# Kernel tuning notes

Measured on AMD Instinct MI355X. Metric: run time of the kernel, lower is better.

The kernel has to match this reference:

```python
import jax, jax.numpy as jnp
import numpy as np

B, S, D, H = 8, 2048, 1024, 1024

def setup_inputs() -> dict:
    key = jax.random.key(0)
    ks = jax.random.split(key, 7)
    scale = 1.0 / np.sqrt(D)
    x = jax.random.normal(ks[0], (B, S, D), dtype=jnp.float32)
    W_q = jax.random.uniform(ks[1], (H, D), jnp.float32, -scale, scale)
    b_q = jax.random.uniform(ks[2], (H,), jnp.float32, -scale, scale)
    W_k = jax.random.uniform(ks[3], (H, D), jnp.float32, -scale, scale)
    b_k = jax.random.uniform(ks[4], (H,), jnp.float32, -scale, scale)
    W_v = jax.random.uniform(ks[5], (H, D), jnp.float32, -scale, scale)
    b_v = jax.random.uniform(ks[6], (H,), jnp.float32, -scale, scale)
    return {"x": x, "W_q": W_q, "b_q": b_q, "W_k": W_k, "b_k": b_k, "W_v": W_v, "b_v": b_v}

def reference(x, W_q, b_q, W_k, b_k, W_v, b_v):
    # Linear layers: y = x @ W.T + b (torch nn.Linear convention)
    q = jnp.einsum('bsd,hd->bsh', x, W_q) + b_q
    k = jnp.einsum('bsd,hd->bsh', x, W_k) + b_k
    v = jnp.einsum('bsd,hd->bsh', x, W_v) + b_v
    score = jnp.einsum('bqh,bkh->bqk', q, k) / jnp.sqrt(jnp.float32(H))
    causal = jnp.tril(jnp.ones((S, S), dtype=bool))  # lower-triangular mask
    score = jnp.where(causal, score, jnp.float32(-1e9))
    attn = jax.nn.softmax(score, axis=-1)
    return jnp.einsum('bqk,bkh->bqh', attn, v)
```

## Files before the change

kernel.cpp:

```cpp
#include <hip/hip_runtime.h>
#include <hip/hip_bf16.h>
#include <cstdint>

#define BB 8
#define SS 2048
#define DD 1024
#define HH 1024

typedef __bf16 bf16x8 __attribute__((ext_vector_type(8)));
typedef float f32x4 __attribute__((ext_vector_type(4)));

#define AS1C(p) ((const __attribute__((address_space(1))) void*)(p))
#define AS3(p)  ((__attribute__((address_space(3))) void*)(p))

__device__ __forceinline__ float bf2f(uint16_t h) {
  union { uint32_t u; float f; } v; v.u = ((uint32_t)h) << 16; return v.f;
}
__device__ __forceinline__ uint16_t f2bf(float f) {
  union { float f; uint32_t u; } v; v.f = f;
  uint32_t u = v.u;
  return (uint16_t)((u + 0x7FFFu + ((u >> 16) & 1u)) >> 16);
}

__global__ void cvt_f32_bf16(const float* __restrict__ src,
                             uint16_t* __restrict__ dst, int n) {
  int i = (blockIdx.x * blockDim.x + threadIdx.x) * 8;
  const int stride = gridDim.x * blockDim.x * 8;
  for (; i < n; i += stride) {
    float4 f0 = *(const float4*)(src + i);
    float4 f1 = *(const float4*)(src + i + 4);
    alignas(16) uint16_t o[8];
    o[0] = f2bf(f0.x); o[1] = f2bf(f0.y); o[2] = f2bf(f0.z); o[3] = f2bf(f0.w);
    o[4] = f2bf(f1.x); o[5] = f2bf(f1.y); o[6] = f2bf(f1.z); o[7] = f2bf(f1.w);
    *(uint4*)(dst + i) = *(const uint4*)o;
  }
}

__global__ void cvt3_f32_bf16(const float* __restrict__ s0, const float* __restrict__ s1,
                              const float* __restrict__ s2, uint16_t* __restrict__ d0,
                              uint16_t* __restrict__ d1, uint16_t* __restrict__ d2, int n) {
  const float* src = (blockIdx.y == 0) ? s0 : (blockIdx.y == 1) ? s1 : s2;
  uint16_t* dst = (blockIdx.y == 0) ? d0 : (blockIdx.y == 1) ? d1 : d2;
  int i = (blockIdx.x * blockDim.x + threadIdx.x) * 8;
  const int stride = gridDim.x * blockDim.x * 8;
  for (; i < n; i += stride) {
    float4 f0 = *(const float4*)(src + i);
    float4 f1 = *(const float4*)(src + i + 4);
    alignas(16) uint16_t o[8];
    o[0] = f2bf(f0.x); o[1] = f2bf(f0.y); o[2] = f2bf(f0.z); o[3] = f2bf(f0.w);
    o[4] = f2bf(f1.x); o[5] = f2bf(f1.y); o[6] = f2bf(f1.z); o[7] = f2bf(f1.w);
    *(uint4*)(dst + i) = *(const uint4*)o;
  }
}

template <int MODE>
__device__ __forceinline__ void gemm_body(const uint16_t* __restrict__ Aroot,
                                          const uint16_t* __restrict__ Broot,
                                          const float* __restrict__ bq,
                                          const float* __restrict__ bk,
                                          const float* __restrict__ bv,
                                          void* __restrict__ out0,
                                          uint16_t* __restrict__ out1,
                                          uint16_t* __restrict__ out2) {
  constexpr int K   = (MODE == 3) ? 2048 : 1024;
  constexpr int LDA = (MODE == 3) ? 2048 : 1024;
  constexpr int LDB = (MODE == 3) ? 2048 : 1024;

  const int tm = (MODE == 3) ? (gridDim.x - 1 - blockIdx.x) : blockIdx.x;
  const int tn = blockIdx.y;
  if constexpr (MODE == 2) { if (tn > tm) return; }

  const uint16_t* A = Aroot;
  const uint16_t* Bp = Broot;
  uint16_t* C16 = (uint16_t*)out0;
  float*    C32 = (float*)out0;
  if constexpr (MODE == 2) {
    size_t z = blockIdx.z;
    A  += z * (size_t)(SS * DD);
    Bp += z * (size_t)(SS * DD);
    C16 += z * (size_t)SS * (size_t)SS;
  }
  if constexpr (MODE == 3) {
    size_t z = blockIdx.z;
    A  += z * (size_t)SS * (size_t)SS;
    Bp += z * (size_t)(HH * SS);
    C32 += z * (size_t)(SS * HH);
  }

  const int m0 = tm * 128, n0 = tn * 128;
  int kmax = K;
  if constexpr (MODE == 3) {
    kmax = (tm + 1) * 128;
    if (kmax > K) kmax = K;
  }

  __shared__ uint16_t As0[128 * 32];
  __shared__ uint16_t As1[128 * 32];
  __shared__ uint16_t Bs0[128 * 32];
  __shared__ uint16_t Bs1[128 * 32];

  const int tid  = threadIdx.x;
  const int lane = tid & 63;
  const int wv   = tid >> 6;
  const int wm   = (wv & 1) * 64;
  const int wn   = (wv >> 1) * 64;

  f32x4 acc[4][4];
#pragma unroll
  for (int i = 0; i < 4; i++)
#pragma unroll
    for (int j = 0; j < 4; j++)
#pragma unroll
      for (int e = 0; e < 4; e++) acc[i][j][e] = 0.f;

  const int lrow = lane >> 2;
  const int lcol = (lane & 3) * 8;
  const int r0   = wv * 32;

  const uint16_t* gA = A + (size_t)(m0 + r0 + lrow) * LDA + lcol;
  const uint16_t* gB = Bp + (size_t)(n0 + r0 + lrow) * LDB + lcol;

  const int fr = lane & 15;
  const int fk = (lane >> 4) * 8;

  for (int k0 = 0; k0 < kmax; k0 += 64) {
    __syncthreads();
    __builtin_amdgcn_global_load_lds(AS1C(gA + k0), AS3(&As0[r0 * 32]), 16, 0, 0);
    __builtin_amdgcn_global_load_lds(AS1C(gA + k0 + 16 * LDA), AS3(&As0[(r0 + 16) * 32]), 16, 0, 0);
    __builtin_amdgcn_global_load_lds(AS1C(gA + k0 + 32), AS3(&As1[r0 * 32]), 16, 0, 0);
    __builtin_amdgcn_global_load_lds(AS1C(gA + k0 + 32 + 16 * LDA), AS3(&As1[(r0 + 16) * 32]), 16, 0, 0);
    __builtin_amdgcn_global_load_lds(AS1C(gB + k0), AS3(&Bs0[r0 * 32]), 16, 0, 0);
    __builtin_amdgcn_global_load_lds(AS1C(gB + k0 + 16 * LDB), AS3(&Bs0[(r0 + 16) * 32]), 16, 0, 0);
    __builtin_amdgcn_global_load_lds(AS1C(gB + k0 + 32), AS3(&Bs1[r0 * 32]), 16, 0, 0);
    __builtin_amdgcn_global_load_lds(AS1C(gB + k0 + 32 + 16 * LDB), AS3(&Bs1[(r0 + 16) * 32]), 16, 0, 0);
    __syncthreads();

    bf16x8 af[4], bfr[4];
#pragma unroll
    for (int i = 0; i < 4; i++)
      af[i] = __builtin_bit_cast(bf16x8, *(const uint4*)&As0[(wm + i * 16 + fr) * 32 + fk]);
#pragma unroll
    for (int j = 0; j < 4; j++)
      bfr[j] = __builtin_bit_cast(bf16x8, *(const uint4*)&Bs0[(wn + j * 16 + fr) * 32 + fk]);
#pragma unroll
    for (int i = 0; i < 4; i++)
#pragma unroll
      for (int j = 0; j < 4; j++)
        acc[i][j] = __builtin_amdgcn_mfma_f32_16x16x32_bf16(af[i], bfr[j], acc[i][j], 0, 0, 0);

#pragma unroll
    for (int i = 0; i < 4; i++)
      af[i] = __builtin_bit_cast(bf16x8, *(const uint4*)&As1[(wm + i * 16 + fr) * 32 + fk]);
#pragma unroll
    for (int j = 0; j < 4; j++)
      bfr[j] = __builtin_bit_cast(bf16x8, *(const uint4*)&Bs1[(wn + j * 16 + fr) * 32 + fk]);
#pragma unroll
    for (int i = 0; i < 4; i++)
#pragma unroll
      for (int j = 0; j < 4; j++)
        acc[i][j] = __builtin_amdgcn_mfma_f32_16x16x32_bf16(af[i], bfr[j], acc[i][j], 0, 0, 0);
  }

  const int cr = (lane >> 4) * 4;
  const int cc = lane & 15;

  if constexpr (MODE == 0) {
    const int sel   = n0 >> 10;
    const int nloc0 = n0 & 1023;
    const float* __restrict__ bsel = (sel == 0) ? bq : (sel == 1) ? bk : bv;
    uint16_t* __restrict__ oQK = (sel == 1) ? out1 : (uint16_t*)out0;
#pragma unroll
    for (int i = 0; i < 4; i++) {
#pragma unroll
      for (int j = 0; j < 4; j++) {
        const int row0 = m0 + wm + i * 16 + cr;
        const int coll = nloc0 + wn + j * 16 + cc;
        const float badd = bsel[coll];
#pragma unroll
        for (int e = 0; e < 4; e++) {
          const float x = acc[i][j][e] + badd;
          const int r = row0 + e;
          if (sel == 2) {
            const int bz = r >> 11;
            const int s  = r & (SS - 1);
            out2[(size_t)bz * (HH * SS) + (size_t)coll * SS + s] = f2bf(x);
          } else {
            oQK[(size_t)r * HH + coll] = f2bf(x);
          }
        }
      }
    }
  } else {
#pragma unroll
    for (int i = 0; i < 4; i++) {
#pragma unroll
      for (int j = 0; j < 4; j++) {
        const int row0 = m0 + wm + i * 16 + cr;
        const int col  = n0 + wn + j * 16 + cc;
#pragma unroll
        for (int e = 0; e < 4; e++) {
          float x = acc[i][j][e];
          const int r = row0 + e;
          if constexpr (MODE == 2) {
            C16[(size_t)r * SS + col] = f2bf(x * 0.03125f);
          } else {
            C32[(size_t)r * HH + col] = x;
          }
        }
      }
    }
  }
}

__launch_bounds__(256, 2)
__global__ void gemm_proj(const uint16_t* __restrict__ A, const uint16_t* __restrict__ B,
                          const float* __restrict__ bq, const float* __restrict__ bk,
                          const float* __restrict__ bv, void* __restrict__ o0,
                          uint16_t* __restrict__ o1, uint16_t* __restrict__ o2) {
  gemm_body<0>(A, B, bq, bk, bv, o0, o1, o2);
}
__launch_bounds__(256, 2)
__global__ void gemm_score(const uint16_t* __restrict__ A, const uint16_t* __restrict__ B,
                           void* __restrict__ o0) {
  gemm_body<2>(A, B, nullptr, nullptr, nullptr, o0, nullptr, nullptr);
}
__launch_bounds__(256, 2)
__global__ void gemm_pv(const uint16_t* __restrict__ A, const uint16_t* __restrict__ B,
                        void* __restrict__ o0) {
  gemm_body<3>(A, B, nullptr, nullptr, nullptr, o0, nullptr, nullptr);
}

__launch_bounds__(256)
__global__ void softmax_causal(uint16_t* __restrict__ Sb) {
  const int rgl = blockIdx.x;
  const int b = rgl >> 11;
  const int i = rgl & (SS - 1);
  uint16_t* row = Sb + (size_t)b * SS * SS + (size_t)i * SS;
  const int t = threadIdx.x;
  const int base = t * 8;
  const int cover = ((i >> 7) + 1) << 7;
  const bool act = base < cover;

  uint4 u; u.x = u.y = u.z = u.w = 0u;
  if (act) u = *(const uint4*)(row + base);
  const uint16_t* hs = (const uint16_t*)&u;
  float x[8];
  float lmax = -3.0e38f;
#pragma unroll
  for (int e = 0; e < 8; e++) {
    float f = bf2f(hs[e]);
    x[e] = (act && base + e <= i) ? f : -3.0e38f;
    lmax = fmaxf(lmax, x[e]);
  }
#pragma unroll
  for (int off = 32; off > 0; off >>= 1)
    lmax = fmaxf(lmax, __shfl_down(lmax, off));

  __shared__ float red[8];
  if ((t & 63) == 0) red[t >> 6] = lmax;
  __syncthreads();
  const float m = fmaxf(fmaxf(red[0], red[1]), fmaxf(red[2], red[3]));

  float lsum = 0.f;
#pragma unroll
  for (int e = 0; e < 8; e++) {
    float p = (act && base + e <= i) ? __expf(x[e] - m) : 0.f;
    x[e] = p;
    lsum += p;
  }
#pragma unroll
  for (int off = 32; off > 0; off >>= 1) lsum += __shfl_down(lsum, off);
  if ((t & 63) == 0) red[4 + (t >> 6)] = lsum;
  __syncthreads();
  const float inv = 1.f / (red[4] + red[5] + red[6] + red[7]);

  if (act) {
    alignas(16) uint16_t o[8];
#pragma unroll
    for (int e = 0; e < 8; e++) o[e] = f2bf(x[e] * inv);
    *(uint4*)(row + base) = *(const uint4*)o;
  }
}

extern "C" void kernel_launch(void* const* d_in, const int* in_sizes, int n_in,
                              void* d_out, int out_size, void* d_ws, size_t ws_size,
                              hipStream_t stream) {
  const float* x  = (const float*)d_in[0];
  const float* Wq = (const float*)d_in[1];
  const float* bq = (const float*)d_in[2];
  const float* Wk = (const float*)d_in[3];
  const float* bk = (const float*)d_in[4];
  const float* Wv = (const float*)d_in[5];
  const float* bv = (const float*)d_in[6];

  uint16_t* ws = (uint16_t*)d_ws;
  const size_t QKV = (size_t)BB * SS * HH;
  uint16_t* Q  = ws;
  uint16_t* Kp = ws + QKV;
  uint16_t* Vt = ws + 2 * QKV;
  uint16_t* Sb = ws + 3 * QKV;
  uint16_t* xb  = Sb;
  uint16_t* Wqb = Sb + QKV;
  uint16_t* Wkb = Wqb + (size_t)HH * DD;
  uint16_t* Wvb = Wkb + (size_t)HH * DD;

  dim3 blk(256);
  const int nx = BB * SS * DD;
  const int nw = HH * DD;
  cvt_f32_bf16<<<dim3(nx / 2048), blk, 0, stream>>>(x, xb, nx);
  cvt3_f32_bf16<<<dim3(nw / 2048, 3), blk, 0, stream>>>(Wq, Wk, Wv, Wqb, Wkb, Wvb, nw);

  gemm_proj<<<dim3(BB * SS / 128, 3 * HH / 128), blk, 0, stream>>>(
      xb, Wqb, bq, bk, bv, Q, Kp, Vt);
  gemm_score<<<dim3(SS / 128, SS / 128, BB), blk, 0, stream>>>(Q, Kp, Sb);
  softmax_causal<<<dim3(BB * SS), blk, 0, stream>>>(Sb);
  gemm_pv<<<dim3(SS / 128, HH / 128, BB), blk, 0, stream>>>(Sb, Vt, d_out);
}
```

Baseline: 419.8 us.

## Fuse causal softmax into score GEMM epilogue and PV normalization

Removes the separate softmax kernel. The score GEMM epilogue now writes exp(score) unnormalized, skipping max subtraction, and accumulates per-row sums with atomics; the PV GEMM divides by the row sum in its epilogue. This saves a full read/write pass over the B×S×S score matrix and one launch. It adds atomic traffic and a memset, and it drops the max subtraction, which risks overflow if the scores are large.

Result: no change. 416.0 us (-0.9%).

```diff
diff --git a/kernel.cpp b/kernel.cpp
--- a/kernel.cpp
+++ b/kernel.cpp
@@ -61,7 +61,8 @@
                                           const float* __restrict__ bv,
                                           void* __restrict__ out0,
                                           uint16_t* __restrict__ out1,
-                                          uint16_t* __restrict__ out2) {
+                                          uint16_t* __restrict__ out2,
+                                          float* __restrict__ rs) {
   constexpr int K   = (MODE == 3) ? 2048 : 1024;
   constexpr int LDA = (MODE == 3) ? 2048 : 1024;
   constexpr int LDB = (MODE == 3) ? 2048 : 1024;
@@ -79,12 +80,14 @@
     A  += z * (size_t)(SS * DD);
     Bp += z * (size_t)(SS * DD);
     C16 += z * (size_t)SS * (size_t)SS;
+    rs += z * (size_t)SS;
   }
   if constexpr (MODE == 3) {
     size_t z = blockIdx.z;
     A  += z * (size_t)SS * (size_t)SS;
     Bp += z * (size_t)(HH * SS);
     C32 += z * (size_t)(SS * HH);
+    rs += z * (size_t)SS;
   }
 
   const int m0 = tm * 128, n0 = tn * 128;
@@ -190,22 +193,40 @@
         }
       }
     }
+  } else if constexpr (MODE == 2) {
+#pragma unroll
+    for (int i = 0; i < 4; i++) {
+#pragma unroll
+      for (int e = 0; e < 4; e++) {
+        const int row = m0 + wm + i * 16 + cr + e;
+        float s = 0.f;
+#pragma unroll
+        for (int j = 0; j < 4; j++) {
+          const int col = n0 + wn + j * 16 + cc;
+          float p = (col <= row) ? __expf(acc[i][j][e] * 0.03125f) : 0.f;
+          const uint16_t pb = f2bf(p);
+          C16[(size_t)row * SS + col] = pb;
+          s += bf2f(pb);
+        }
+        s += __shfl_xor(s, 1);
+        s += __shfl_xor(s, 2);
+        s += __shfl_xor(s, 4);
+        s += __shfl_xor(s, 8);
+        if (cc == 0) atomicAdd(&rs[row], s);
+      }
+    }
   } else {
 #pragma unroll
     for (int i = 0; i < 4; i++) {
+      const int rr = m0 + wm + i * 16 + cr;
+      const float4 rv = *(const float4*)&rs[rr];
+      const float inv[4] = {1.f / rv.x, 1.f / rv.y, 1.f / rv.z, 1.f / rv.w};
 #pragma unroll
       for (int j = 0; j < 4; j++) {
-        const int row0 = m0 + wm + i * 16 + cr;
-        const int col  = n0 + wn + j * 16 + cc;
+        const int col = n0 + wn + j * 16 + cc;
 #pragma unroll
         for (int e = 0; e < 4; e++) {
-          float x = acc[i][j][e];
-          const int r = row0 + e;
-          if constexpr (MODE == 2) {
-            C16[(size_t)r * SS + col] = f2bf(x * 0.03125f);
-          } else {
-            C32[(size_t)r * HH + col] = x;
-          }
+          C32[(size_t)(rr + e) * HH + col] = acc[i][j][e] * inv[e];
         }
       }
     }
@@ -217,69 +238,17 @@
                           const float* __restrict__ bq, const float* __restrict__ bk,
                           const float* __restrict__ bv, void* __restrict__ o0,
                           uint16_t* __restrict__ o1, uint16_t* __restrict__ o2) {
-  gemm_body<0>(A, B, bq, bk, bv, o0, o1, o2);
+  gemm_body<0>(A, B, bq, bk, bv, o0, o1, o2, nullptr);
 }
 __launch_bounds__(256, 2)
 __global__ void gemm_score(const uint16_t* __restrict__ A, const uint16_t* __restrict__ B,
-                           void* __restrict__ o0) {
-  gemm_body<2>(A, B, nullptr, nullptr, nullptr, o0, nullptr, nullptr);
+                           void* __restrict__ o0, float* __restrict__ rs) {
+  gemm_body<2>(A, B, nullptr, nullptr, nullptr, o0, nullptr, nullptr, rs);
 }
 __launch_bounds__(256, 2)
 __global__ void gemm_pv(const uint16_t* __restrict__ A, const uint16_t* __restrict__ B,
-                        void* __restrict__ o0) {
-  gemm_body<3>(A, B, nullptr, nullptr, nullptr, o0, nullptr, nullptr);
-}
-
-__launch_bounds__(256)
-__global__ void softmax_causal(uint16_t* __restrict__ Sb) {
-  const int rgl = blockIdx.x;
-  const int b = rgl >> 11;
-  const int i = rgl & (SS - 1);
-  uint16_t* row = Sb + (size_t)b * SS * SS + (size_t)i * SS;
-  const int t = threadIdx.x;
-  const int base = t * 8;
-  const int cover = ((i >> 7) + 1) << 7;
-  const bool act = base < cover;
-
-  uint4 u; u.x = u.y = u.z = u.w = 0u;
-  if (act) u = *(const uint4*)(row + base);
-  const uint16_t* hs = (const uint16_t*)&u;
-  float x[8];
-  float lmax = -3.0e38f;
-#pragma unroll
-  for (int e = 0; e < 8; e++) {
-    float f = bf2f(hs[e]);
-    x[e] = (act && base + e <= i) ? f : -3.0e38f;
-    lmax = fmaxf(lmax, x[e]);
-  }
-#pragma unroll
-  for (int off = 32; off > 0; off >>= 1)
-    lmax = fmaxf(lmax, __shfl_down(lmax, off));
-
-  __shared__ float red[8];
-  if ((t & 63) == 0) red[t >> 6] = lmax;
-  __syncthreads();
-  const float m = fmaxf(fmaxf(red[0], red[1]), fmaxf(red[2], red[3]));
-
-  float lsum = 0.f;
-#pragma unroll
-  for (int e = 0; e < 8; e++) {
-    float p = (act && base + e <= i) ? __expf(x[e] - m) : 0.f;
-    x[e] = p;
-    lsum += p;
-  }
-#pragma unroll
-  for (int off = 32; off > 0; off >>= 1) lsum += __shfl_down(lsum, off);
-  if ((t & 63) == 0) red[4 + (t >> 6)] = lsum;
-  __syncthreads();
-  const float inv = 1.f / (red[4] + red[5] + red[6] + red[7]);
-
-  if (act) {
-    alignas(16) uint16_t o[8];
-#pragma unroll
-    for (int e = 0; e < 8; e++) o[e] = f2bf(x[e] * inv);
-    *(uint4*)(row + base) = *(const uint4*)o;
-  }
+                        void* __restrict__ o0, float* __restrict__ rs) {
+  gemm_body<3>(A, B, nullptr, nullptr, nullptr, o0, nullptr, nullptr, rs);
 }
 
 extern "C" void kernel_launch(void* const* d_in, const int* in_sizes, int n_in,
@@ -303,16 +272,17 @@
   uint16_t* Wqb = Sb + QKV;
   uint16_t* Wkb = Wqb + (size_t)HH * DD;
   uint16_t* Wvb = Wkb + (size_t)HH * DD;
+  float* rowsum = (float*)(Sb + (size_t)BB * SS * SS);
 
   dim3 blk(256);
   const int nx = BB * SS * DD;
   const int nw = HH * DD;
+  hipMemsetAsync(rowsum, 0, (size_t)BB * SS * sizeof(float), stream);
   cvt_f32_bf16<<<dim3(nx / 2048), blk, 0, stream>>>(x, xb, nx);
   cvt3_f32_bf16<<<dim3(nw / 2048, 3), blk, 0, stream>>>(Wq, Wk, Wv, Wqb, Wkb, Wvb, nw);
 
   gemm_proj<<<dim3(BB * SS / 128, 3 * HH / 128), blk, 0, stream>>>(
       xb, Wqb, bq, bk, bv, Q, Kp, Vt);
-  gemm_score<<<dim3(SS / 128, SS / 128, BB), blk, 0, stream>>>(Q, Kp, Sb);
-  softmax_causal<<<dim3(BB * SS), blk, 0, stream>>>(Sb);
-  gemm_pv<<<dim3(SS / 128, HH / 128, BB), blk, 0, stream>>>(Sb, Vt, d_out);
-}
+  gemm_score<<<dim3(SS / 128, SS / 128, BB), blk, 0, stream>>>(Q, Kp, Sb, rowsum);
+  gemm_pv<<<dim3(SS / 128, HH / 128, BB), blk, 0, stream>>>(Sb, Vt, d_out, rowsum);
+}
```
